# Kernel tuning notes

Measured on AMD Instinct MI355X. Metric: run time of the kernel, lower is better.

Reference implementation:

```python
import jax, jax.numpy as jnp
import numpy as np

B, T, IN, H = 32, 256, 64, 128
TOP_K = 5
TRUNC = 100   # truncate_length: detach h,c every TRUNC steps
EPS = 1e-7
NEG = -1e9


def setup_inputs() -> dict:
    key = jax.random.key(0)
    ks = jax.random.split(key, 6)
    s = 1.0 / np.sqrt(H)  # torch LSTMCell default init bound
    xav = float(1.414 * np.sqrt(6.0 / (2 * H + 1)))  # xavier_uniform gain=1.414
    return {
        "x": jax.random.normal(ks[0], (B, T, IN), jnp.float32),
        "W_ih": jax.random.uniform(ks[1], (4 * H, IN), jnp.float32, -s, s),
        "W_hh": jax.random.uniform(ks[2], (4 * H, H), jnp.float32, -s, s),
        "b_ih": jax.random.uniform(ks[3], (4 * H,), jnp.float32, -s, s),
        "b_hh": jax.random.uniform(ks[4], (4 * H,), jnp.float32, -s, s),
        "w_t": jax.random.uniform(ks[5], (2 * H, 1), jnp.float32, -xav, xav),
    }


def _lstm_cell(x_t, h, c, W_ih, W_hh, b_ih, b_hh):
    # torch gate order: i, f, g, o
    g = x_t @ W_ih.T + h @ W_hh.T + (b_ih + b_hh)
    i, f, gg, o = jnp.split(g, 4, axis=-1)
    c = jax.nn.sigmoid(f) * c + jax.nn.sigmoid(i) * jnp.tanh(gg)
    h = jax.nn.sigmoid(o) * jnp.tanh(c)
    return h, c


def reference(x, W_ih, W_hh, b_ih, b_hh, w_t):
    Bv, Tv, _ = x.shape
    Hh = W_hh.shape[1]
    # score = w_t . tanh(cat(h_t, h_old)) splits additively since tanh is elementwise
    w_a = w_t[:Hh, 0]
    w_b = w_t[Hh:, 0]
    pos = jnp.arange(Tv + 1)

    def step(carry, inp):
        h, c, h_old = carry          # h_old: [B, T+1, H], slot 0 = initial zeros
        i, x_t = inp
        det = ((i + 1) % TRUNC) == 0
        h = jnp.where(det, jax.lax.stop_gradient(h), h)
        c = jnp.where(det, jax.lax.stop_gradient(c), c)
        h, c = _lstm_cell(x_t, h, c, W_ih, W_hh, b_ih, b_hh)
        rem = i + 1                  # remember_size
        mask = pos < rem             # [T+1] valid memory slots
        # attention scores over stored states
        s = (jnp.tanh(h) @ w_a)[:, None] + jnp.tanh(h_old) @ w_b  # [B, T+1]
        s_valid = jnp.where(mask[None, :], s, NEG)
        delta = jax.lax.top_k(s_valid, TOP_K)[0][:, -1] + EPS
        w_sp = jnp.clip(s_valid - delta[:, None], 0.0)
        w_sp = w_sp / (w_sp.sum(axis=1, keepdims=True) + EPS)
        # Sparse_attention returns raw scores when remember_size <= top_k
        attn_w = jnp.where(rem <= TOP_K, s, w_sp)
        attn_c = jnp.einsum('bt,bth->bh', jnp.where(mask[None, :], attn_w, 0.0), h_old)
        h = h + attn_c
        h_old = jax.lax.dynamic_update_slice(h_old, h[:, None, :], (0, rem, 0))
        return (h, c, h_old), (attn_c, attn_w)

    h0 = jnp.zeros((Bv, Hh), x.dtype)
    c0 = jnp.zeros((Bv, Hh), x.dtype)
    buf0 = jnp.zeros((Bv, Tv + 1, Hh), x.dtype)
    xs = (jnp.arange(Tv), jnp.swapaxes(x, 0, 1))
    _, (attn_c_all, attn_w_all) = jax.lax.scan(step, (h0, c0, buf0), xs)
    # module returns last step's (attn_c, out_attn_w); final remember_size == T
    return attn_c_all[-1], attn_w_all[-1][:, :Tv, None]
```

## Files before the change

### kernel.cpp

```cpp
#include <hip/hip_runtime.h>
#include <math.h>

#define NEGF -1000000000.0f
#define EPSF 1e-7f


__device__ __forceinline__ float fsigmoid(float x) {
  return 1.0f / (1.0f + __expf(-x));
}
__device__ __forceinline__ float ftanh(float x) {
  return 1.0f - 2.0f / (1.0f + __expf(2.0f * x));
}

__device__ __forceinline__ float wave_allsum(float v) {
#if __has_builtin(__builtin_amdgcn_update_dpp) && __has_builtin(__builtin_amdgcn_readlane)
  float f = v;
#define DPPSTEP(ctrl, rmask) { \
    int t = __builtin_amdgcn_update_dpp(0, __builtin_bit_cast(int, f), \
                                        ctrl, rmask, 0xf, true); \
    f += __builtin_bit_cast(float, t); }
  DPPSTEP(0x111, 0xf)
  DPPSTEP(0x112, 0xf)
  DPPSTEP(0x114, 0xf)
  DPPSTEP(0x118, 0xf)
  DPPSTEP(0x142, 0xa)
  DPPSTEP(0x143, 0x8)
#undef DPPSTEP
  return __builtin_bit_cast(float,
      __builtin_amdgcn_readlane(__builtin_bit_cast(int, f), 63));
#else
  for (int off = 1; off < 64; off <<= 1) v += __shfl_xor(v, off, 64);
  return v;
#endif
}

__global__ __launch_bounds__(512) void xw_kernel(
    const float* __restrict__ x, const float* __restrict__ W_ih,
    const float* __restrict__ b_ih, const float* __restrict__ b_hh,
    float* __restrict__ xw)
{
  const int t0 = blockIdx.x * 32;
  const int b  = blockIdx.y;
  const int g  = threadIdx.x;

  __shared__ float sx[32 * 64];
  ((float4*)sx)[threadIdx.x] =
      ((const float4*)(x + (size_t)(b * 256 + t0) * 64))[threadIdx.x];

  const float4* wr = (const float4*)(W_ih + (size_t)g * 64);
  float4 w0 = wr[0],  w1 = wr[1],  w2 = wr[2],  w3 = wr[3],
         w4 = wr[4],  w5 = wr[5],  w6 = wr[6],  w7 = wr[7],
         w8 = wr[8],  w9 = wr[9],  w10 = wr[10], w11 = wr[11],
         w12 = wr[12], w13 = wr[13], w14 = wr[14], w15 = wr[15];
  const float bias = b_ih[g] + b_hh[g];
  __syncthreads();

  float* dst = xw + (size_t)(b * 256 + t0) * 512 + g;
  for (int tt = 0; tt < 32; ++tt) {
    const float4* xr = (const float4*)(sx + tt * 64);
    float a0 = 0.0f, a1 = 0.0f, a2 = 0.0f, a3 = 0.0f;
#define XSTEP(j) { float4 hv = xr[j]; \
    a0 = fmaf(w##j.x, hv.x, a0); a1 = fmaf(w##j.y, hv.y, a1); \
    a2 = fmaf(w##j.z, hv.z, a2); a3 = fmaf(w##j.w, hv.w, a3); }
    XSTEP(0) XSTEP(1) XSTEP(2) XSTEP(3) XSTEP(4) XSTEP(5) XSTEP(6) XSTEP(7)
    XSTEP(8) XSTEP(9) XSTEP(10) XSTEP(11) XSTEP(12) XSTEP(13) XSTEP(14) XSTEP(15)
#undef XSTEP
    dst[(size_t)tt * 512] = (a0 + a1) + (a2 + a3) + bias;
  }
}

__global__
__attribute__((amdgpu_flat_work_group_size(1024, 1024), amdgpu_waves_per_eu(4, 4)))
void lstm_attn(
    const float* __restrict__ xw, const float* __restrict__ W_hh,
    const float* __restrict__ w_t, float* __restrict__ out)
{
  const int b   = blockIdx.x;
  const int tid = threadIdx.x;
  const int l   = tid & 63;
  const int wid = tid >> 6;
  const int p   = tid & 255;
  const int q   = tid >> 8;
  const int gA  = p;
  const int gB  = p + 256;

  __shared__ float ho[257 * 128];
  __shared__ float sh_part[4 * 512];
  __shared__ float sh_d[8];

  const float4* pA = (const float4*)(W_hh + (size_t)gA * 128 + (q << 5));
  const float4* pB = (const float4*)(W_hh + (size_t)gB * 128 + (q << 5));
  float4 wA0 = pA[0], wA1 = pA[1], wA2 = pA[2], wA3 = pA[3],
         wA4 = pA[4], wA5 = pA[5], wA6 = pA[6], wA7 = pA[7];
  float4 wB0 = pB[0], wB1 = pB[1], wB2 = pB[2], wB3 = pB[3],
         wB4 = pB[4], wB5 = pB[5], wB6 = pB[6], wB7 = pB[7];

  const int j0 = 2 * l, j1 = 2 * l + 1;
  float c0 = 0.0f, c1 = 0.0f;
  float wa0 = 0.0f, wa1 = 0.0f, wb0 = 0.0f, wb1 = 0.0f;
  float t5v0 = 0.0f, t5v1 = NEGF, t5v2 = NEGF, t5v3 = NEGF, t5v4 = NEGF;
  int   t5i0 = 0, t5i1 = 0, t5i2 = 0, t5i3 = 0;
  float gn0 = 0.0f, gn1 = 0.0f, gn2 = 0.0f, gn3 = 0.0f;
  int   ofs0 = 0, ofs1 = 0, ofs2 = 0, ofs3 = 0;

  if (wid == 0) {
    wa0 = w_t[j0];       wa1 = w_t[j1];
    wb0 = w_t[128 + j0]; wb1 = w_t[128 + j1];
    *(float2*)(ho + j0) = make_float2(0.0f, 0.0f);
    __builtin_amdgcn_s_setprio(1);
  }
  if (tid == 0) sh_d[0] = 0.0f;
  __syncthreads();

  const float* xwb = xw + (size_t)b * 256 * 512;
  float xcurA = 0.0f, xcurB = 0.0f;
  if (q == 0) { xcurA = xwb[gA]; xcurB = xwb[gB]; }

  for (int i = 0; i < 256; ++i) {
    const int rem = i + 1;
    float hn0 = 0.0f, hn1 = 0.0f;

    float aA0 = xcurA, aA1 = 0.0f, aB0 = xcurB, aB1 = 0.0f;
    if (q == 0 && i < 255) {
      xcurA = xwb[(size_t)(i + 1) * 512 + gA];
      xcurB = xwb[(size_t)(i + 1) * 512 + gB];
    }
    const float4* hh4 = (const float4*)(ho + i * 128 + (q << 5));
#define LSTEP(j) { float4 hv = hh4[j]; \
    aA0 = fmaf(wA##j.x, hv.x, aA0); aA1 = fmaf(wA##j.y, hv.y, aA1); \
    aA0 = fmaf(wA##j.z, hv.z, aA0); aA1 = fmaf(wA##j.w, hv.w, aA1); \
    aB0 = fmaf(wB##j.x, hv.x, aB0); aB1 = fmaf(wB##j.y, hv.y, aB1); \
    aB0 = fmaf(wB##j.z, hv.z, aB0); aB1 = fmaf(wB##j.w, hv.w, aB1); }
    LSTEP(0) LSTEP(1) LSTEP(2) LSTEP(3) LSTEP(4) LSTEP(5) LSTEP(6) LSTEP(7)
#undef LSTEP
    sh_part[(q << 9) + gA] = aA0 + aA1;
    sh_part[(q << 9) + gB] = aB0 + aB1;

    float2 hv0, hv1, hv2, hv3;
    if (wid == 0 && i >= 5) {
      hv0 = *(const float2*)(ho + ofs0);
      hv1 = *(const float2*)(ho + ofs1);
      hv2 = *(const float2*)(ho + ofs2);
      hv3 = *(const float2*)(ho + ofs3);
    }
    __syncthreads();

    if (wid == 0) {
#define GSUM(base) ({ \
      float2 x0 = ((const float2*)(sh_part        + (base)))[l]; \
      float2 x1 = ((const float2*)(sh_part +  512 + (base)))[l]; \
      float2 x2 = ((const float2*)(sh_part + 1024 + (base)))[l]; \
      float2 x3 = ((const float2*)(sh_part + 1536 + (base)))[l]; \
      float2 r; r.x = (x0.x + x1.x) + (x2.x + x3.x); \
      r.y = (x0.y + x1.y) + (x2.y + x3.y); r; })
      float2 Pi = GSUM(0), Pf = GSUM(128), Pg = GSUM(256), Po = GSUM(384);
#undef GSUM
      c0 = fsigmoid(Pf.x) * c0 + fsigmoid(Pi.x) * ftanh(Pg.x);
      c1 = fsigmoid(Pf.y) * c1 + fsigmoid(Pi.y) * ftanh(Pg.y);
      float hc0 = fsigmoid(Po.x) * ftanh(c0);
      float hc1 = fsigmoid(Po.y) * ftanh(c1);

      float at0, at1;
      if (i >= 5) {
        at0 = gn0 * hv0.x;            at1 = gn0 * hv0.y;
        at0 = fmaf(gn1, hv1.x, at0);  at1 = fmaf(gn1, hv1.y, at1);
        at0 = fmaf(gn2, hv2.x, at0);  at1 = fmaf(gn2, hv2.y, at1);
        at0 = fmaf(gn3, hv3.x, at0);  at1 = fmaf(gn3, hv3.y, at1);
      } else {
        float a = wave_allsum(ftanh(hc0) * wa0 + ftanh(hc1) * wa1);
        at0 = 0.0f; at1 = 0.0f;
        for (int t = 0; t <= i; ++t) {
          float s = a + sh_d[t];
          float2 hv = *(const float2*)(ho + t * 128 + j0);
          at0 = fmaf(s, hv.x, at0);
          at1 = fmaf(s, hv.y, at1);
        }
      }
      hn0 = hc0 + at0; hn1 = hc1 + at1;
      *(float2*)(ho + rem * 128 + j0) = make_float2(hn0, hn1);
      if (i == 255) {
        out[b * 128 + j0] = at0; out[b * 128 + j1] = at1;
        #pragma unroll
        for (int m = 0; m < 4; ++m) {
          int t = l + 64 * m;
          float val = 0.0f;
          if (t == t5i0) val = gn0;
          if (t == t5i1) val = gn1;
          if (t == t5i2) val = gn2;
          if (t == t5i3) val = gn3;
          out[4096 + b * 256 + t] = val;
        }
      }
    }
    __syncthreads();

    if (wid == 0 && i < 255) {
      float dn = wave_allsum(ftanh(hn0) * wb0 + ftanh(hn1) * wb1);
      if (l == 0 && i < 4) sh_d[rem] = dn;
      float v = dn; int vi = rem;
      if (v > t5v0) { float tv = t5v0; int ti = t5i0; t5v0 = v; t5i0 = vi; v = tv; vi = ti; }
      if (v > t5v1) { float tv = t5v1; int ti = t5i1; t5v1 = v; t5i1 = vi; v = tv; vi = ti; }
      if (v > t5v2) { float tv = t5v2; int ti = t5i2; t5v2 = v; t5i2 = vi; v = tv; vi = ti; }
      if (v > t5v3) { float tv = t5v3; int ti = t5i3; t5v3 = v; t5i3 = vi; v = tv; vi = ti; }
      if (v > t5v4) { t5v4 = v; }
      float g0 = fmaxf(t5v0 - t5v4 - EPSF, 0.0f);
      float g1 = fmaxf(t5v1 - t5v4 - EPSF, 0.0f);
      float g2 = fmaxf(t5v2 - t5v4 - EPSF, 0.0f);
      float g3 = fmaxf(t5v3 - t5v4 - EPSF, 0.0f);
      float inv = 1.0f / (((g0 + g1) + (g2 + g3)) + EPSF);
      gn0 = g0 * inv; gn1 = g1 * inv; gn2 = g2 * inv; gn3 = g3 * inv;
      ofs0 = (t5i0 << 7) + j0; ofs1 = (t5i1 << 7) + j0;
      ofs2 = (t5i2 << 7) + j0; ofs3 = (t5i3 << 7) + j0;
    }
  }
}

extern "C" void kernel_launch(void* const* d_in, const int* in_sizes, int n_in,
                              void* d_out, int out_size, void* d_ws, size_t ws_size,
                              hipStream_t stream) {
  const float* x    = (const float*)d_in[0];
  const float* W_ih = (const float*)d_in[1];
  const float* W_hh = (const float*)d_in[2];
  const float* b_ih = (const float*)d_in[3];
  const float* b_hh = (const float*)d_in[4];
  const float* w_t  = (const float*)d_in[5];
  float* out = (float*)d_out;

  float* xw = (float*)d_ws;

  xw_kernel<<<dim3(8, 32), 512, 0, stream>>>(x, W_ih, b_ih, b_hh, xw);
  lstm_attn<<<dim3(32), 1024, 0, stream>>>(xw, W_hh, w_t, out);
}
```

Baseline: 412.7 us.

## Shrink recurrent LSTM block to 4 waves with 8 gate rows per thread

```diff
diff --git a/kernel.cpp b/kernel.cpp
--- a/kernel.cpp
+++ b/kernel.cpp
@@ -34,43 +34,55 @@
 #endif
 }
 
-__global__ __launch_bounds__(512) void xw_kernel(
+__global__
+__attribute__((amdgpu_flat_work_group_size(256, 256), amdgpu_waves_per_eu(2)))
+void xw_kernel(
     const float* __restrict__ x, const float* __restrict__ W_ih,
     const float* __restrict__ b_ih, const float* __restrict__ b_hh,
     float* __restrict__ xw)
 {
-  const int t0 = blockIdx.x * 32;
+  const int t0 = blockIdx.x * 16;
   const int b  = blockIdx.y;
   const int g  = threadIdx.x;
 
-  __shared__ float sx[32 * 64];
+  __shared__ float sx[16 * 64];
   ((float4*)sx)[threadIdx.x] =
       ((const float4*)(x + (size_t)(b * 256 + t0) * 64))[threadIdx.x];
 
-  const float4* wr = (const float4*)(W_ih + (size_t)g * 64);
-  float4 w0 = wr[0],  w1 = wr[1],  w2 = wr[2],  w3 = wr[3],
-         w4 = wr[4],  w5 = wr[5],  w6 = wr[6],  w7 = wr[7],
-         w8 = wr[8],  w9 = wr[9],  w10 = wr[10], w11 = wr[11],
-         w12 = wr[12], w13 = wr[13], w14 = wr[14], w15 = wr[15];
-  const float bias = b_ih[g] + b_hh[g];
+  const float4* wra = (const float4*)(W_ih + (size_t)g * 64);
+  const float4* wrb = (const float4*)(W_ih + (size_t)(g + 256) * 64);
+  float4 wa0 = wra[0],  wa1 = wra[1],  wa2 = wra[2],  wa3 = wra[3],
+         wa4 = wra[4],  wa5 = wra[5],  wa6 = wra[6],  wa7 = wra[7],
+         wa8 = wra[8],  wa9 = wra[9],  wa10 = wra[10], wa11 = wra[11],
+         wa12 = wra[12], wa13 = wra[13], wa14 = wra[14], wa15 = wra[15];
+  float4 wb0 = wrb[0],  wb1 = wrb[1],  wb2 = wrb[2],  wb3 = wrb[3],
+         wb4 = wrb[4],  wb5 = wrb[5],  wb6 = wrb[6],  wb7 = wrb[7],
+         wb8 = wrb[8],  wb9 = wrb[9],  wb10 = wrb[10], wb11 = wrb[11],
+         wb12 = wrb[12], wb13 = wrb[13], wb14 = wrb[14], wb15 = wrb[15];
+  const float biasA = b_ih[g] + b_hh[g];
+  const float biasB = b_ih[g + 256] + b_hh[g + 256];
   __syncthreads();
 
   float* dst = xw + (size_t)(b * 256 + t0) * 512 + g;
-  for (int tt = 0; tt < 32; ++tt) {
+  for (int tt = 0; tt < 16; ++tt) {
     const float4* xr = (const float4*)(sx + tt * 64);
     float a0 = 0.0f, a1 = 0.0f, a2 = 0.0f, a3 = 0.0f;
+    float c0 = 0.0f, c1 = 0.0f, c2 = 0.0f, c3 = 0.0f;
 #define XSTEP(j) { float4 hv = xr[j]; \
-    a0 = fmaf(w##j.x, hv.x, a0); a1 = fmaf(w##j.y, hv.y, a1); \
-    a2 = fmaf(w##j.z, hv.z, a2); a3 = fmaf(w##j.w, hv.w, a3); }
+    a0 = fmaf(wa##j.x, hv.x, a0); a1 = fmaf(wa##j.y, hv.y, a1); \
+    a2 = fmaf(wa##j.z, hv.z, a2); a3 = fmaf(wa##j.w, hv.w, a3); \
+    c0 = fmaf(wb##j.x, hv.x, c0); c1 = fmaf(wb##j.y, hv.y, c1); \
+    c2 = fmaf(wb##j.z, hv.z, c2); c3 = fmaf(wb##j.w, hv.w, c3); }
     XSTEP(0) XSTEP(1) XSTEP(2) XSTEP(3) XSTEP(4) XSTEP(5) XSTEP(6) XSTEP(7)
     XSTEP(8) XSTEP(9) XSTEP(10) XSTEP(11) XSTEP(12) XSTEP(13) XSTEP(14) XSTEP(15)
 #undef XSTEP
-    dst[(size_t)tt * 512] = (a0 + a1) + (a2 + a3) + bias;
+    dst[(size_t)tt * 512]       = (a0 + a1) + (a2 + a3) + biasA;
+    dst[(size_t)tt * 512 + 256] = (c0 + c1) + (c2 + c3) + biasB;
   }
 }
 
 __global__
-__attribute__((amdgpu_flat_work_group_size(1024, 1024), amdgpu_waves_per_eu(4, 4)))
+__attribute__((amdgpu_flat_work_group_size(256, 256), amdgpu_waves_per_eu(1, 1)))
 void lstm_attn(
     const float* __restrict__ xw, const float* __restrict__ W_hh,
     const float* __restrict__ w_t, float* __restrict__ out)
@@ -78,22 +90,20 @@
   const int b   = blockIdx.x;
   const int tid = threadIdx.x;
   const int l   = tid & 63;
-  const int wid = tid >> 6;
-  const int p   = tid & 255;
-  const int q   = tid >> 8;
-  const int gA  = p;
-  const int gB  = p + 256;
+  const int q   = tid >> 6;
+  const int gb  = l << 3;
 
   __shared__ float ho[257 * 128];
   __shared__ float sh_part[4 * 512];
   __shared__ float sh_d[8];
 
-  const float4* pA = (const float4*)(W_hh + (size_t)gA * 128 + (q << 5));
-  const float4* pB = (const float4*)(W_hh + (size_t)gB * 128 + (q << 5));
-  float4 wA0 = pA[0], wA1 = pA[1], wA2 = pA[2], wA3 = pA[3],
-         wA4 = pA[4], wA5 = pA[5], wA6 = pA[6], wA7 = pA[7];
-  float4 wB0 = pB[0], wB1 = pB[1], wB2 = pB[2], wB3 = pB[3],
-         wB4 = pB[4], wB5 = pB[5], wB6 = pB[6], wB7 = pB[7];
+#define LOADW(g) \
+  const float4* pw##g = (const float4*)(W_hh + (size_t)(gb + g) * 128 + (q << 5)); \
+  float4 w##g##_0 = pw##g[0], w##g##_1 = pw##g[1], w##g##_2 = pw##g[2], \
+         w##g##_3 = pw##g[3], w##g##_4 = pw##g[4], w##g##_5 = pw##g[5], \
+         w##g##_6 = pw##g[6], w##g##_7 = pw##g[7];
+  LOADW(0) LOADW(1) LOADW(2) LOADW(3) LOADW(4) LOADW(5) LOADW(6) LOADW(7)
+#undef LOADW
 
   const int j0 = 2 * l, j1 = 2 * l + 1;
   float c0 = 0.0f, c1 = 0.0f;
@@ -103,41 +113,54 @@
   float gn0 = 0.0f, gn1 = 0.0f, gn2 = 0.0f, gn3 = 0.0f;
   int   ofs0 = 0, ofs1 = 0, ofs2 = 0, ofs3 = 0;
 
-  if (wid == 0) {
+  if (q == 0) {
     wa0 = w_t[j0];       wa1 = w_t[j1];
     wb0 = w_t[128 + j0]; wb1 = w_t[128 + j1];
     *(float2*)(ho + j0) = make_float2(0.0f, 0.0f);
-    __builtin_amdgcn_s_setprio(1);
   }
   if (tid == 0) sh_d[0] = 0.0f;
   __syncthreads();
 
   const float* xwb = xw + (size_t)b * 256 * 512;
-  float xcurA = 0.0f, xcurB = 0.0f;
-  if (q == 0) { xcurA = xwb[gA]; xcurB = xwb[gB]; }
+  float4 xc0 = make_float4(0.f, 0.f, 0.f, 0.f);
+  float4 xc1 = make_float4(0.f, 0.f, 0.f, 0.f);
+  if (q == 0) {
+    xc0 = ((const float4*)(xwb + gb))[0];
+    xc1 = ((const float4*)(xwb + gb))[1];
+  }
 
   for (int i = 0; i < 256; ++i) {
     const int rem = i + 1;
     float hn0 = 0.0f, hn1 = 0.0f;
 
-    float aA0 = xcurA, aA1 = 0.0f, aB0 = xcurB, aB1 = 0.0f;
+    float A0x = xc0.x, A0y = 0.0f, A1x = xc0.y, A1y = 0.0f;
+    float A2x = xc0.z, A2y = 0.0f, A3x = xc0.w, A3y = 0.0f;
+    float A4x = xc1.x, A4y = 0.0f, A5x = xc1.y, A5y = 0.0f;
+    float A6x = xc1.z, A6y = 0.0f, A7x = xc1.w, A7y = 0.0f;
     if (q == 0 && i < 255) {
-      xcurA = xwb[(size_t)(i + 1) * 512 + gA];
-      xcurB = xwb[(size_t)(i + 1) * 512 + gB];
+      xc0 = ((const float4*)(xwb + (size_t)(i + 1) * 512 + gb))[0];
+      xc1 = ((const float4*)(xwb + (size_t)(i + 1) * 512 + gb))[1];
     }
     const float4* hh4 = (const float4*)(ho + i * 128 + (q << 5));
-#define LSTEP(j) { float4 hv = hh4[j]; \
-    aA0 = fmaf(wA##j.x, hv.x, aA0); aA1 = fmaf(wA##j.y, hv.y, aA1); \
-    aA0 = fmaf(wA##j.z, hv.z, aA0); aA1 = fmaf(wA##j.w, hv.w, aA1); \
-    aB0 = fmaf(wB##j.x, hv.x, aB0); aB1 = fmaf(wB##j.y, hv.y, aB1); \
-    aB0 = fmaf(wB##j.z, hv.z, aB0); aB1 = fmaf(wB##j.w, hv.w, aB1); }
-    LSTEP(0) LSTEP(1) LSTEP(2) LSTEP(3) LSTEP(4) LSTEP(5) LSTEP(6) LSTEP(7)
-#undef LSTEP
-    sh_part[(q << 9) + gA] = aA0 + aA1;
-    sh_part[(q << 9) + gB] = aB0 + aB1;
+#define FGA(g, kk) \
+    A##g##x = fmaf(w##g##_##kk.x, hv.x, A##g##x); \
+    A##g##y = fmaf(w##g##_##kk.y, hv.y, A##g##y); \
+    A##g##x = fmaf(w##g##_##kk.z, hv.z, A##g##x); \
+    A##g##y = fmaf(w##g##_##kk.w, hv.w, A##g##y);
+#define KSTEP(kk) { float4 hv = hh4[kk]; \
+    FGA(0, kk) FGA(1, kk) FGA(2, kk) FGA(3, kk) \
+    FGA(4, kk) FGA(5, kk) FGA(6, kk) FGA(7, kk) }
+    KSTEP(0) KSTEP(1) KSTEP(2) KSTEP(3) KSTEP(4) KSTEP(5) KSTEP(6) KSTEP(7)
+#undef KSTEP
+#undef FGA
+    {
+      float4* sp4 = (float4*)(sh_part + (q << 9) + (l << 3));
+      sp4[0] = make_float4(A0x + A0y, A1x + A1y, A2x + A2y, A3x + A3y);
+      sp4[1] = make_float4(A4x + A4y, A5x + A5y, A6x + A6y, A7x + A7y);
+    }
 
     float2 hv0, hv1, hv2, hv3;
-    if (wid == 0 && i >= 5) {
+    if (q == 0 && i >= 5) {
       hv0 = *(const float2*)(ho + ofs0);
       hv1 = *(const float2*)(ho + ofs1);
       hv2 = *(const float2*)(ho + ofs2);
@@ -145,7 +168,7 @@
     }
     __syncthreads();
 
-    if (wid == 0) {
+    if (q == 0) {
 #define GSUM(base) ({ \
       float2 x0 = ((const float2*)(sh_part        + (base)))[l]; \
       float2 x1 = ((const float2*)(sh_part +  512 + (base)))[l]; \
@@ -194,7 +217,7 @@
     }
     __syncthreads();
 
-    if (wid == 0 && i < 255) {
+    if (q == 0 && i < 255) {
       float dn = wave_allsum(ftanh(hn0) * wb0 + ftanh(hn1) * wb1);
       if (l == 0 && i < 4) sh_d[rem] = dn;
       float v = dn; int vi = rem;
@@ -228,6 +251,6 @@
 
   float* xw = (float*)d_ws;
 
-  xw_kernel<<<dim3(8, 32), 512, 0, stream>>>(x, W_ih, b_ih, b_hh, xw);
-  lstm_attn<<<dim3(32), 1024, 0, stream>>>(xw, W_hh, w_t, out);
-}
+  xw_kernel<<<dim3(16, 32), 256, 0, stream>>>(x, W_ih, b_ih, b_hh, xw);
+  lstm_attn<<<dim3(32), 256, 0, stream>>>(xw, W_hh, w_t, out);
+}
```

Result: slower. 503.3 us (+21.9%).
